# Kernel tuning notes

Measured on AMD Instinct MI355X. Metric: run time of the kernel, lower is better.

Reference implementation:

```python
import jax, jax.numpy as jnp
import numpy as np

# static conv hyperparams (match init_kwargs)
KH = KW = 3
SH = SW = 1
PH = PW = 1
DH = DW = 1


def _unfold(x):
    """torch F.unfold equivalent with constant pad value -1.
    x: (N, C, H, W) -> patches (N, C*KH*KW, L), feature order (C, kh, kw)."""
    N, C, H, W = x.shape
    H_out = (H + 2 * PH - DH * (KH - 1) - 1) // SH + 1
    W_out = (W + 2 * PW - DW * (KW - 1) - 1) // SW + 1
    padded = jnp.pad(x, ((0, 0), (0, 0), (PH, PH), (PW, PW)), constant_values=-1.0)
    cols = [
        padded[:, :, ih * DH: ih * DH + SH * H_out: SH,
                     iw * DW: iw * DW + SW * W_out: SW]
        for ih in range(KH) for iw in range(KW)
    ]
    patches = jnp.stack(cols, axis=2)  # (N, C, KH*KW, H_out, W_out)
    return patches.reshape(N, C * KH * KW, H_out * W_out), H_out, W_out


def _maj3_tree(x):
    """Recursive 3-way majority-gate tree reduction over the last axis.
    x: (..., K) with K a power of 3. MAJ3Fn math: xs=(x+1)/2;
    r = ab+ac+bc-2abc; y = 2r-1."""
    while x.shape[-1] > 1:
        k = x.shape[-1] // 3
        g = x.reshape(x.shape[:-1] + (k, 3))
        s = (g + 1.0) * 0.5
        a, b, c = s[..., 0], s[..., 1], s[..., 2]
        r = a * b + a * c + b * c - 2.0 * a * b * c
        x = 2.0 * r - 1.0
    return x[..., 0]


def setup_inputs() -> dict:
    key = jax.random.key(0)
    k1, k2 = jax.random.split(key)
    x = jax.random.normal(k1, (8, 27, 32, 32), dtype=jnp.float32)
    # kaiming_uniform-ish scale for (OC=27, C=27, 3, 3)
    fan_in = 27 * 3 * 3
    bound = np.sqrt(6.0 / fan_in)
    weight = jax.random.uniform(k2, (27, 27, 3, 3), dtype=jnp.float32,
                                minval=-bound, maxval=bound)
    return {"x": x, "weight": weight}


def reference(x, weight):
    N = x.shape[0]
    OC = weight.shape[0]
    patches, H_out, W_out = _unfold(x)          # (N, K, L), K = C*KH*KW
    wf = weight.reshape(OC, -1)                  # (OC, K)
    prod = patches[:, None, :, :] * wf[None, :, :, None]  # (N, OC, K, L)
    prod = jnp.moveaxis(prod, 2, -1)             # (N, OC, L, K)
    out = _maj3_tree(prod)                       # (N, OC, L)
    return out.reshape(N, OC, H_out, W_out)
```

## Files before the change

### kernel.cpp

```cpp
#include <hip/hip_runtime.h>


#define HH 32
#define WW 32
#define CC 27
#define OCC 27

typedef float v2f __attribute__((ext_vector_type(2)));

__device__ __forceinline__ v2f splat2(float s) { v2f r; r.x = s; r.y = s; return r; }

__device__ __forceinline__ v2f maj3v(v2f a, v2f b, v2f c) {
    v2f ab = a * b;
    v2f t  = __builtin_elementwise_fma(splat2(-2.0f), ab, a + b);
    return __builtin_elementwise_fma(c, t, ab);
}

__device__ __forceinline__ float maj3(float a, float b, float c) {
    float ab = a * b;
    float t  = fmaf(-2.0f, ab, a + b);
    return fmaf(c, t, ab);
}

__global__ __launch_bounds__(768) void sconv_maj_kernel(
    const float* __restrict__ x, const float* __restrict__ w, float* __restrict__ out)
{
    __shared__ float smem[27 * 6 * 36 + 4 * 128 * 3];
    float* tile = smem;
    float* part = smem + 27 * 6 * 36;

    const int b    = blockIdx.x;
    const int rg   = b & 7;
    const int rest = b >> 3;
    const int ocg  = rest % 7;
    const int n    = rest / 7;
    const int tid  = threadIdx.x;

    const float* __restrict__ xb = x + n * (CC * HH * WW);

    {
#pragma unroll
        for (int it = 0; it < 2; ++it) {
            const int s = tid + it * 768;
            if (s < 162 * 8) {
                const int R  = s >> 3;
                const int q  = s & 7;
                const int c  = R / 6;
                const int tr = R - c * 6;
                const int ih = rg * 4 + tr - 1;
                float4 v = make_float4(-0.5f, -0.5f, -0.5f, -0.5f);
                if ((unsigned)ih < 32u) {
                    const float4 u = *(const float4*)(xb + c * (HH * WW) + ih * WW + q * 4);
                    v.x = 0.5f * u.x; v.y = 0.5f * u.y;
                    v.z = 0.5f * u.z; v.w = 0.5f * u.w;
                }
                float* d = &tile[R * 36 + 1 + q * 4];
                d[0] = v.x; d[1] = v.y; d[2] = v.z; d[3] = v.w;
            }
        }
        if (tid < 324) {
            const int R = tid >> 1;
            tile[R * 36 + ((tid & 1) ? 33 : 0)] = -0.5f;
        }
    }
    __syncthreads();

    const int wavei    = __builtin_amdgcn_readfirstlane(tid >> 6);
    const int oc_local = wavei / 3;
    const int sub3     = wavei - oc_local * 3;
    const int oc       = ocg * 4 + oc_local;
    const int lt  = tid & 63;
    const int pr  = lt >> 4;
    const int ow0 = (lt & 15) << 1;

    if (oc < OCC) {
        const float* __restrict__ wp = w + oc * 243 + sub3 * 81;

        __builtin_amdgcn_s_setprio(1);
        v2f l4[3];
#pragma unroll
        for (int c2 = 0; c2 < 3; ++c2) {
            v2f l3[3];
#pragma unroll
            for (int c1 = 0; c1 < 3; ++c1) {
                const int c  = sub3 * 9 + c2 * 3 + c1;
                const int cw = c2 * 3 + c1;
                const float* trow = &tile[(c * 6 + pr) * 36 + ow0];
                v2f rv[3];
#pragma unroll
                for (int kh = 0; kh < 3; ++kh) {
                    const float2 u0 = *(const float2*)(trow + kh * 36);
                    const float2 u1 = *(const float2*)(trow + kh * 36 + 2);
                    const float w0 = wp[cw * 9 + kh * 3 + 0];
                    const float w1 = wp[cw * 9 + kh * 3 + 1];
                    const float w2 = wp[cw * 9 + kh * 3 + 2];
                    v2f t0; t0.x = u0.x; t0.y = u0.y;
                    v2f t1; t1.x = u0.y; t1.y = u1.x;
                    v2f t2; t2.x = u1.x; t2.y = u1.y;
                    v2f s0 = __builtin_elementwise_fma(t0, splat2(w0), splat2(0.5f));
                    v2f s1 = __builtin_elementwise_fma(t1, splat2(w1), splat2(0.5f));
                    v2f s2 = __builtin_elementwise_fma(t2, splat2(w2), splat2(0.5f));
                    rv[kh] = maj3v(s0, s1, s2);
                }
                l3[c1] = maj3v(rv[0], rv[1], rv[2]);
            }
            l4[c2] = maj3v(l3[0], l3[1], l3[2]);
        }
        const v2f pv = maj3v(l4[0], l4[1], l4[2]);
        __builtin_amdgcn_s_setprio(0);

        const int base = (oc_local * 128 + pr * 32 + ow0) * 3 + sub3;
        part[base]     = pv.x;
        part[base + 3] = pv.y;
    }
    __syncthreads();

    if (tid < 512) {
        const int ocl = tid >> 7;
        const int px  = tid & 127;
        const int oc2 = ocg * 4 + ocl;
        if (oc2 < OCC) {
            const int b0 = (ocl * 128 + px) * 3;
            const float y = fmaf(2.0f, maj3(part[b0], part[b0 + 1], part[b0 + 2]), -1.0f);
            const int oh = rg * 4 + (px >> 5);
            const int ow = px & 31;
            out[(((n * OCC + oc2) * HH) + oh) * WW + ow] = y;
        }
    }
}

extern "C" void kernel_launch(void* const* d_in, const int* in_sizes, int n_in,
                              void* d_out, int out_size, void* d_ws, size_t ws_size,
                              hipStream_t stream) {
    const float* x = (const float*)d_in[0];
    const float* w = (const float*)d_in[1];
    float* out = (float*)d_out;
    sconv_maj_kernel<<<dim3(8 * 7 * 8), dim3(768), 0, stream>>>(x, w, out);
}
```

Baseline: 60.53 us.

## Assign one full output channel per wave, drop cross-wave partial reduction

Each wave now reduces all 27 input channels for one output channel, replacing the split of one channel across three waves that met in shared memory. Blocks shrink to 448 threads covering 7 output channels, and the grid goes from 448 to 256 blocks. This removes the second barrier, the partial-result shared buffer and the final reduction pass, and lets each thread write a float2 straight to global memory. In exchange, each wave carries a serial chain three times longer, there are fewer waves in flight, and the input tile is loaded into fewer, larger blocks, which may hurt latency hiding. The s_setprio hints are also dropped.

```diff
diff --git a/kernel.cpp b/kernel.cpp
--- a/kernel.cpp
+++ b/kernel.cpp
@@ -16,116 +16,92 @@
     return __builtin_elementwise_fma(c, t, ab);
 }
 
-__device__ __forceinline__ float maj3(float a, float b, float c) {
-    float ab = a * b;
-    float t  = fmaf(-2.0f, ab, a + b);
-    return fmaf(c, t, ab);
-}
-
-__global__ __launch_bounds__(768) void sconv_maj_kernel(
+__global__ __launch_bounds__(448) void sconv_maj_kernel(
     const float* __restrict__ x, const float* __restrict__ w, float* __restrict__ out)
 {
-    __shared__ float smem[27 * 6 * 36 + 4 * 128 * 3];
-    float* tile = smem;
-    float* part = smem + 27 * 6 * 36;
+    __shared__ float tile[27 * 6 * 36];
 
-    const int b    = blockIdx.x;
-    const int rg   = b & 7;
-    const int rest = b >> 3;
-    const int ocg  = rest % 7;
-    const int n    = rest / 7;
-    const int tid  = threadIdx.x;
+    const int b   = blockIdx.x;
+    const int rg  = b & 7;
+    const int ocg = (b >> 3) & 3;
+    const int n   = b >> 5;
+    const int tid = threadIdx.x;
 
     const float* __restrict__ xb = x + n * (CC * HH * WW);
 
-    {
 #pragma unroll
-        for (int it = 0; it < 2; ++it) {
-            const int s = tid + it * 768;
-            if (s < 162 * 8) {
-                const int R  = s >> 3;
-                const int q  = s & 7;
-                const int c  = R / 6;
-                const int tr = R - c * 6;
-                const int ih = rg * 4 + tr - 1;
-                float4 v = make_float4(-0.5f, -0.5f, -0.5f, -0.5f);
-                if ((unsigned)ih < 32u) {
-                    const float4 u = *(const float4*)(xb + c * (HH * WW) + ih * WW + q * 4);
-                    v.x = 0.5f * u.x; v.y = 0.5f * u.y;
-                    v.z = 0.5f * u.z; v.w = 0.5f * u.w;
-                }
-                float* d = &tile[R * 36 + 1 + q * 4];
-                d[0] = v.x; d[1] = v.y; d[2] = v.z; d[3] = v.w;
+    for (int it = 0; it < 3; ++it) {
+        const int s = tid + it * 448;
+        if (s < 162 * 8) {
+            const int R  = s >> 3;
+            const int q  = s & 7;
+            const int c  = R / 6;
+            const int tr = R - c * 6;
+            const int ih = rg * 4 + tr - 1;
+            float4 v = make_float4(-0.5f, -0.5f, -0.5f, -0.5f);
+            if ((unsigned)ih < 32u) {
+                const float4 u = *(const float4*)(xb + c * (HH * WW) + ih * WW + q * 4);
+                v.x = 0.5f * u.x; v.y = 0.5f * u.y;
+                v.z = 0.5f * u.z; v.w = 0.5f * u.w;
             }
+            float* d = &tile[R * 36 + 1 + q * 4];
+            d[0] = v.x; d[1] = v.y; d[2] = v.z; d[3] = v.w;
         }
-        if (tid < 324) {
-            const int R = tid >> 1;
-            tile[R * 36 + ((tid & 1) ? 33 : 0)] = -0.5f;
-        }
+    }
+    if (tid < 324) {
+        const int R = tid >> 1;
+        tile[R * 36 + ((tid & 1) ? 33 : 0)] = -0.5f;
     }
     __syncthreads();
 
-    const int wavei    = __builtin_amdgcn_readfirstlane(tid >> 6);
-    const int oc_local = wavei / 3;
-    const int sub3     = wavei - oc_local * 3;
-    const int oc       = ocg * 4 + oc_local;
+    const int wavei = __builtin_amdgcn_readfirstlane(tid >> 6);
+    const int oc    = ocg * 7 + wavei;
     const int lt  = tid & 63;
     const int pr  = lt >> 4;
     const int ow0 = (lt & 15) << 1;
 
     if (oc < OCC) {
-        const float* __restrict__ wp = w + oc * 243 + sub3 * 81;
+        const float* __restrict__ wp = w + oc * 243;
 
-        __builtin_amdgcn_s_setprio(1);
-        v2f l4[3];
+        v2f l5[3];
 #pragma unroll
-        for (int c2 = 0; c2 < 3; ++c2) {
-            v2f l3[3];
+        for (int c3 = 0; c3 < 3; ++c3) {
+            v2f l4[3];
 #pragma unroll
-            for (int c1 = 0; c1 < 3; ++c1) {
-                const int c  = sub3 * 9 + c2 * 3 + c1;
-                const int cw = c2 * 3 + c1;
-                const float* trow = &tile[(c * 6 + pr) * 36 + ow0];
-                v2f rv[3];
+            for (int c2 = 0; c2 < 3; ++c2) {
+                v2f l3[3];
 #pragma unroll
-                for (int kh = 0; kh < 3; ++kh) {
-                    const float2 u0 = *(const float2*)(trow + kh * 36);
-                    const float2 u1 = *(const float2*)(trow + kh * 36 + 2);
-                    const float w0 = wp[cw * 9 + kh * 3 + 0];
-                    const float w1 = wp[cw * 9 + kh * 3 + 1];
-                    const float w2 = wp[cw * 9 + kh * 3 + 2];
-                    v2f t0; t0.x = u0.x; t0.y = u0.y;
-                    v2f t1; t1.x = u0.y; t1.y = u1.x;
-                    v2f t2; t2.x = u1.x; t2.y = u1.y;
-                    v2f s0 = __builtin_elementwise_fma(t0, splat2(w0), splat2(0.5f));
-                    v2f s1 = __builtin_elementwise_fma(t1, splat2(w1), splat2(0.5f));
-                    v2f s2 = __builtin_elementwise_fma(t2, splat2(w2), splat2(0.5f));
-                    rv[kh] = maj3v(s0, s1, s2);
+                for (int c1 = 0; c1 < 3; ++c1) {
+                    const int c = c3 * 9 + c2 * 3 + c1;
+                    const float* trow = &tile[(c * 6 + pr) * 36 + ow0];
+                    v2f rv[3];
+#pragma unroll
+                    for (int kh = 0; kh < 3; ++kh) {
+                        const float2 u0 = *(const float2*)(trow + kh * 36);
+                        const float2 u1 = *(const float2*)(trow + kh * 36 + 2);
+                        const float w0 = wp[c * 9 + kh * 3 + 0];
+                        const float w1 = wp[c * 9 + kh * 3 + 1];
+                        const float w2 = wp[c * 9 + kh * 3 + 2];
+                        v2f t0; t0.x = u0.x; t0.y = u0.y;
+                        v2f t1; t1.x = u0.y; t1.y = u1.x;
+                        v2f t2; t2.x = u1.x; t2.y = u1.y;
+                        v2f s0 = __builtin_elementwise_fma(t0, splat2(w0), splat2(0.5f));
+                        v2f s1 = __builtin_elementwise_fma(t1, splat2(w1), splat2(0.5f));
+                        v2f s2 = __builtin_elementwise_fma(t2, splat2(w2), splat2(0.5f));
+                        rv[kh] = maj3v(s0, s1, s2);
+                    }
+                    l3[c1] = maj3v(rv[0], rv[1], rv[2]);
                 }
-                l3[c1] = maj3v(rv[0], rv[1], rv[2]);
+                l4[c2] = maj3v(l3[0], l3[1], l3[2]);
             }
-            l4[c2] = maj3v(l3[0], l3[1], l3[2]);
+            l5[c3] = maj3v(l4[0], l4[1], l4[2]);
         }
-        const v2f pv = maj3v(l4[0], l4[1], l4[2]);
-        __builtin_amdgcn_s_setprio(0);
+        const v2f f = maj3v(l5[0], l5[1], l5[2]);
+        const v2f y = __builtin_elementwise_fma(splat2(2.0f), f, splat2(-1.0f));
 
-        const int base = (oc_local * 128 + pr * 32 + ow0) * 3 + sub3;
-        part[base]     = pv.x;
-        part[base + 3] = pv.y;
-    }
-    __syncthreads();
-
-    if (tid < 512) {
-        const int ocl = tid >> 7;
-        const int px  = tid & 127;
-        const int oc2 = ocg * 4 + ocl;
-        if (oc2 < OCC) {
-            const int b0 = (ocl * 128 + px) * 3;
-            const float y = fmaf(2.0f, maj3(part[b0], part[b0 + 1], part[b0 + 2]), -1.0f);
-            const int oh = rg * 4 + (px >> 5);
-            const int ow = px & 31;
-            out[(((n * OCC + oc2) * HH) + oh) * WW + ow] = y;
-        }
+        const int oh = rg * 4 + pr;
+        float* op = out + (((n * OCC + oc) * HH) + oh) * WW + ow0;
+        *(float2*)op = make_float2(y.x, y.y);
     }
 }
 
@@ -135,5 +111,5 @@
     const float* x = (const float*)d_in[0];
     const float* w = (const float*)d_in[1];
     float* out = (float*)d_out;
-    sconv_maj_kernel<<<dim3(8 * 7 * 8), dim3(768), 0, stream>>>(x, w, out);
+    sconv_maj_kernel<<<dim3(8 * 4 * 8), dim3(448), 0, stream>>>(x, w, out);
 }
```

New measurement: 62.95 us. 1.04x slower.
